# Kernel optimization log

Measured on AMD Instinct MI355X. Metric: run time of the kernel, lower is better.

Reference implementation:

```python
import jax, jax.numpy as jnp
import numpy as np

B, S, D, H = 4, 4096, 1024, 1024  # batch, seq, token_dim (d+1), hidden_dim
WIN, STRIDE, GLOB = 256, 128, 16
EPS = 1e-5
SCALE = 1.0 / np.sqrt(H).astype(np.float32)


def build_sparse_causal_mask(seq_len):
    i = jnp.arange(seq_len)[:, None]
    j = jnp.arange(seq_len)[None, :]
    causal = j <= i
    allowed = causal & ((i - j) < WIN)          # local window
    allowed = allowed | (((i - j) % STRIDE == 0) & causal)  # strided
    allowed = allowed | ((j < GLOB) & causal)   # global tokens
    return allowed  # [S, S] bool


def layer_norm(x, g, b):
    m = jnp.mean(x, axis=-1, keepdims=True)
    v = jnp.mean(jnp.square(x - m), axis=-1, keepdims=True)
    return (x - m) * jax.lax.rsqrt(v + EPS) * g + b


def setup_inputs() -> dict:
    key = jax.random.key(0)
    ks = jax.random.split(key, 5)
    gain = 0.01
    # xavier_uniform bound for square [H,D] matrices
    def xavier(k, shape):
        bound = gain * np.sqrt(6.0 / (shape[0] + shape[1]))
        return jax.random.uniform(k, shape, jnp.float32, -bound, bound)
    return {
        "tokens": jax.random.normal(ks[0], (B, S, D), jnp.float32),
        "Wq": xavier(ks[1], (D, H)),
        "Wk": xavier(ks[2], (D, H)),
        "Wv": xavier(ks[3], (D, D)),
        "Wo": xavier(ks[4], (D, D)),
        "g1": jnp.ones((D,), jnp.float32),
        "b1": jnp.zeros((D,), jnp.float32),
        "g2": jnp.ones((D,), jnp.float32),
        "b2": jnp.zeros((D,), jnp.float32),
    }


def reference(tokens, Wq, Wk, Wv, Wo, g1, b1, g2, b2):
    x = layer_norm(tokens, g1, b1)                    # [B,S,D]
    Q = jnp.einsum("bsd,dh->bsh", x, Wq)              # [B,S,H]
    K = jnp.einsum("bsd,dh->bsh", x, Wk)
    V = jnp.einsum("bsd,de->bse", x, Wv)              # [B,S,D]
    scores = jnp.einsum("bqh,bkh->bqk", Q, K) * SCALE  # [B,S,S]
    allowed = build_sparse_causal_mask(S)
    scores = jnp.where(allowed, scores, -jnp.inf)
    weights = jax.nn.softmax(scores, axis=-1)
    attn = jnp.einsum("bqk,bkd->bqd", weights, V)     # [B,S,D]
    out = tokens + jnp.einsum("bsd,de->bse", attn, Wo) * 0.1
    return layer_norm(out, g2, b2)
```

## Files before the change

kernel.cpp:

```cpp
#include <hip/hip_runtime.h>

#define S_LEN   4096
#define D_DIM   1024
#define WIN_    256
#define STRIDE_ 128
#define GLOB_   16
#define SCALE_F 0.03125f
#define EPS_F   1e-5f

typedef __bf16 bf16x8 __attribute__((ext_vector_type(8)));
typedef float  f32x4  __attribute__((ext_vector_type(4)));

__device__ __forceinline__ float b2f(unsigned short u) {
    union { unsigned int i; float f; } c; c.i = ((unsigned int)u) << 16; return c.f;
}
__device__ __forceinline__ unsigned short f2bf(float f) {
    union { float f; unsigned int i; } c; c.f = f;
    unsigned int u = c.i;
    u += 0x7fffu + ((u >> 16) & 1u);
    return (unsigned short)(u >> 16);
}

__device__ __forceinline__ void gld_lds16(const void* g, void* l) {
    __builtin_amdgcn_global_load_lds(
        (const __attribute__((address_space(1))) unsigned int*)g,
        (__attribute__((address_space(3))) unsigned int*)l, 16, 0, 0);
}

__device__ __forceinline__ float blk_sum(float v, float* red, int tid) {
    int lane = tid & 63, wv = tid >> 6;
    #pragma unroll
    for (int m = 32; m >= 1; m >>= 1) v += __shfl_xor(v, m, 64);
    __syncthreads();
    if (lane == 0) red[wv] = v;
    __syncthreads();
    return red[0] + red[1] + red[2] + red[3];
}

__global__ __launch_bounds__(256) void ln_full_kernel(
    const float* __restrict__ in, float* __restrict__ mu, float* __restrict__ rs,
    const float* __restrict__ g, const float* __restrict__ bb,
    unsigned short* __restrict__ xb) {
    __shared__ float red[4];
    int row = blockIdx.x, tid = threadIdx.x;
    size_t off = (size_t)row * D_DIM + tid * 4;
    float4 r = *(const float4*)(in + off);
    float s = blk_sum(r.x + r.y + r.z + r.w, red, tid);
    float mean = s * (1.0f / 1024.0f);
    float d0 = r.x - mean, d1 = r.y - mean, d2 = r.z - mean, d3 = r.w - mean;
    float s2 = blk_sum(d0*d0 + d1*d1 + d2*d2 + d3*d3, red, tid);
    float rstd = rsqrtf(s2 * (1.0f / 1024.0f) + EPS_F);
    if (tid == 0) { mu[row] = mean; rs[row] = rstd; }
    float4 gr = *(const float4*)(g  + tid * 4);
    float4 br = *(const float4*)(bb + tid * 4);
    ushort4 o;
    o.x = f2bf(d0 * rstd * gr.x + br.x);
    o.y = f2bf(d1 * rstd * gr.y + br.y);
    o.z = f2bf(d2 * rstd * gr.z + br.z);
    o.w = f2bf(d3 * rstd * gr.w + br.w);
    *(ushort4*)(xb + off) = o;
}

__global__ __launch_bounds__(256) void ln2_inplace_kernel(
    float* __restrict__ data, const float* __restrict__ g,
    const float* __restrict__ bb) {
    __shared__ float red[4];
    int row = blockIdx.x, tid = threadIdx.x;
    size_t off = (size_t)row * D_DIM + tid * 4;
    float4 v = *(const float4*)(data + off);
    float s = blk_sum(v.x + v.y + v.z + v.w, red, tid);
    float mean = s * (1.0f / 1024.0f);
    float d0 = v.x - mean, d1 = v.y - mean, d2 = v.z - mean, d3 = v.w - mean;
    float s2 = blk_sum(d0*d0 + d1*d1 + d2*d2 + d3*d3, red, tid);
    float rstd = rsqrtf(s2 * (1.0f / 1024.0f) + EPS_F);
    float4 gr = *(const float4*)(g  + tid * 4);
    float4 br = *(const float4*)(bb + tid * 4);
    float4 o;
    o.x = d0 * rstd * gr.x + br.x;
    o.y = d1 * rstd * gr.y + br.y;
    o.z = d2 * rstd * gr.z + br.z;
    o.w = d3 * rstd * gr.w + br.w;
    *(float4*)(data + off) = o;
}

__global__ __launch_bounds__(256) void transpose_cvt(
    const float* __restrict__ in, unsigned short* __restrict__ outp) {
    __shared__ unsigned short tile[32][33];
    int tid = threadIdx.x;
    int tx = tid & 31, ty = tid >> 5;
    int bx = blockIdx.x * 32, by = blockIdx.y * 32;
    #pragma unroll
    for (int r = 0; r < 32; r += 8)
        tile[ty + r][tx] = f2bf(in[(size_t)(by + ty + r) * 1024 + bx + tx]);
    __syncthreads();
    #pragma unroll
    for (int r = 0; r < 32; r += 8)
        outp[(size_t)(bx + ty + r) * 1024 + by + tx] = tile[tx][ty + r];
}

__global__ __launch_bounds__(256) void transpose1024(
    const unsigned short* __restrict__ in, unsigned short* __restrict__ outp) {
    __shared__ unsigned short tile[32][33];
    int tid = threadIdx.x;
    int tx = tid & 31, ty = tid >> 5;
    int bx = blockIdx.x * 32, by = blockIdx.y * 32;
    #pragma unroll
    for (int r = 0; r < 32; r += 8)
        tile[ty + r][tx] = in[(size_t)(by + ty + r) * 1024 + bx + tx];
    __syncthreads();
    #pragma unroll
    for (int r = 0; r < 32; r += 8)
        outp[(size_t)(bx + ty + r) * 1024 + by + tx] = tile[tx][ty + r];
}

__global__ __launch_bounds__(256) void transln16_kernel(
    const float* __restrict__ tok, const float* __restrict__ mu,
    const float* __restrict__ rs, const float* __restrict__ g,
    const float* __restrict__ bb, unsigned short* __restrict__ X16) {
    __shared__ unsigned short Lt[32][36];
    int tid = threadIdx.x;
    int tx = tid & 31, ty = tid >> 5;
    int s0 = blockIdx.x * 32;
    int n0 = blockIdx.y * 32;
    int b  = blockIdx.z;
    float gv = g[n0 + tx], bv = bb[n0 + tx];
    #pragma unroll
    for (int r = 0; r < 32; r += 8) {
        int grow = (b << 12) + s0 + ty + r;
        float v = tok[(size_t)grow * 1024 + n0 + tx];
        Lt[tx][ty + r] = f2bf((v - mu[grow]) * rs[grow] * gv + bv);
    }
    __syncthreads();
    int tt  = tid >> 6;
    int sTl = tt >> 1, nTl = tt & 1;
    int idx = tid & 63;
    int nl  = idx >> 2, so4 = (idx & 3) << 2;
    uint2 v = *(const uint2*)&Lt[nTl * 16 + nl][sTl * 16 + so4];
    size_t off = (size_t)b * 4194304 +
        (((size_t)(((s0 >> 4) + sTl) * 64 + (n0 >> 4) + nTl)) << 8) +
        (nl << 4) + so4;
    *(uint2*)(X16 + off) = v;
}

__global__ __launch_bounds__(256) void gemm_small(
    const float* __restrict__ A32, const float* __restrict__ W32,
    unsigned short* __restrict__ C16) {
    const int K = 1024, N = 1024;
    __shared__ __align__(16) unsigned short As[64][40];
    __shared__ __align__(16) unsigned short Bs[64][40];
    int tid  = threadIdx.x;
    int lane = tid & 63, wv = tid >> 6;
    int lm   = lane & 15, quad = lane >> 4;
    int m0 = blockIdx.y * 64, n0 = blockIdx.x * 64;
    int srow = tid >> 2, scg = tid & 3;
    int bk   = tid >> 3, bn  = (tid & 7) * 8;

    f32x4 acc[4] = {};
    for (int k0 = 0; k0 < K; k0 += 32) {
        const float* ap = A32 + (size_t)(m0 + srow) * K + k0 + scg * 8;
        float4 p = *(const float4*)(ap);
        float4 q = *(const float4*)(ap + 4);
        union { uint4 u; unsigned short s[8]; } w;
        w.s[0]=f2bf(p.x); w.s[1]=f2bf(p.y); w.s[2]=f2bf(p.z); w.s[3]=f2bf(p.w);
        w.s[4]=f2bf(q.x); w.s[5]=f2bf(q.y); w.s[6]=f2bf(q.z); w.s[7]=f2bf(q.w);
        *(uint4*)&As[srow][scg * 8] = w.u;

        const float* wp = W32 + (size_t)(k0 + bk) * N + n0 + bn;
        float4 a = *(const float4*)wp, b = *(const float4*)(wp + 4);
        float wvv[8] = {a.x,a.y,a.z,a.w,b.x,b.y,b.z,b.w};
        #pragma unroll
        for (int e = 0; e < 8; ++e) Bs[bn + e][bk] = f2bf(wvv[e]);
        __syncthreads();
        bf16x8 af = *(const bf16x8*)&As[wv * 16 + lm][quad * 8];
        #pragma unroll
        for (int t = 0; t < 4; ++t) {
            bf16x8 bfr = *(const bf16x8*)&Bs[t * 16 + lm][quad * 8];
            acc[t] = __builtin_amdgcn_mfma_f32_16x16x32_bf16(af, bfr, acc[t], 0, 0, 0);
        }
        __syncthreads();
    }
    #pragma unroll
    for (int t = 0; t < 4; ++t) {
        int col = n0 + t * 16 + lm;
        #pragma unroll
        for (int r = 0; r < 4; ++r) {
            int row = m0 + wv * 16 + quad * 4 + r;
            C16[(size_t)row * N + col] = f2bf(acc[t][r]);
        }
    }
}

template <bool EPI>
__global__ __launch_bounds__(256) void gemm128(
    const unsigned short* __restrict__ A, const unsigned short* __restrict__ BT,
    unsigned short* __restrict__ C16, float* __restrict__ Cres,
    const float* __restrict__ tok) {
    const int K = 1024, N = 1024;
    __shared__ __align__(16) unsigned short As[4096];
    __shared__ __align__(16) unsigned short Bs[4096];
    int tid = threadIdx.x, lane = tid & 63, wv = tid >> 6;
    int lm = lane & 15, quad = lane >> 4;
    int wr = wv >> 1, wc = wv & 1;
    int flat = blockIdx.y * 8 + blockIdx.x;
    int logical = ((flat & 7) << 7) | (flat >> 3);
    int m0 = (logical >> 3) * 128, n0 = (logical & 7) * 128;

    f32x4 acc[4][4] = {};

    const unsigned short* ga0 = A  + (size_t)(m0 + lane) * K + wv * 8;
    const unsigned short* ga1 = A  + (size_t)(m0 + 64 + lane) * K + wv * 8;
    const unsigned short* gb0 = BT + (size_t)(n0 + lane) * K + wv * 8;
    const unsigned short* gb1 = BT + (size_t)(n0 + 64 + lane) * K + wv * 8;
    unsigned short* la0 = &As[wv * 1024 + lane * 8];
    unsigned short* la1 = &As[wv * 1024 + 512 + lane * 8];
    unsigned short* lb0 = &Bs[wv * 1024 + lane * 8];
    unsigned short* lb1 = &Bs[wv * 1024 + 512 + lane * 8];

    for (int k0 = 0; k0 < K; k0 += 32) {
        gld_lds16(ga0 + k0, la0);
        gld_lds16(ga1 + k0, la1);
        gld_lds16(gb0 + k0, lb0);
        gld_lds16(gb1 + k0, lb1);
        __syncthreads();
        bf16x8 af[4], bfr[4];
        #pragma unroll
        for (int t = 0; t < 4; ++t) {
            af[t]  = *(const bf16x8*)&As[quad * 1024 + (wr * 64 + t * 16 + lm) * 8];
            bfr[t] = *(const bf16x8*)&Bs[quad * 1024 + (wc * 64 + t * 16 + lm) * 8];
        }
        #pragma unroll
        for (int mt = 0; mt < 4; ++mt)
            #pragma unroll
            for (int nt = 0; nt < 4; ++nt)
                acc[mt][nt] = __builtin_amdgcn_mfma_f32_16x16x32_bf16(
                    af[mt], bfr[nt], acc[mt][nt], 0, 0, 0);
        __syncthreads();
    }
    #pragma unroll
    for (int mt = 0; mt < 4; ++mt) {
        #pragma unroll
        for (int nt = 0; nt < 4; ++nt) {
            int col = n0 + wc * 64 + nt * 16 + lm;
            #pragma unroll
            for (int r = 0; r < 4; ++r) {
                int row = m0 + wr * 64 + mt * 16 + quad * 4 + r;
                size_t idx = (size_t)row * N + col;
                if (EPI) Cres[idx] = tok[idx] + 0.1f * acc[mt][nt][r];
                else     C16[idx]  = f2bf(acc[mt][nt][r]);
            }
        }
    }
}

#define NT_MAX 48
#define SCROW  776
__global__ __launch_bounds__(256) void attn16_kernel(
    const unsigned short* __restrict__ Q, const unsigned short* __restrict__ K,
    const unsigned short* __restrict__ XT, unsigned short* __restrict__ Ao) {
    __shared__ __align__(16) unsigned short Ps[16 * SCROW];
    int tid = threadIdx.x, lane = tid & 63, wv = tid >> 6;
    int lm = lane & 15, quad = lane >> 4;
    int bxr = blockIdx.x;
    int xcd = bxr & 7;
    int sl  = bxr >> 3;
    int batch = xcd >> 1;
    int ptyp  = xcd & 1;
    int t = ptyp ? (64 + sl)
                 : ((sl < 64) ? sl : (128 + sl));
    int bx = batch * 256 + t;
    int b  = bx >> 8;
    int i0 = (bx & 255) << 4;
    int rowbase = (b << 12) + i0;
    int wlo = i0 - 256; if (wlo < 0) wlo = 0;
    int nwin = ((i0 - wlo) >> 4) + 1;
    int tmax = (i0 - 16) / 128;
    int nstr = tmax - 2; if (nstr < 0) nstr = 0;
    int nglob = (wlo > 0) ? 1 : 0;
    int ntiles = nwin + nstr + nglob;
    int ntp = (ntiles + 3) & ~3;

    const unsigned short* Qg = Q + (size_t)(rowbase + lm) * 1024 + quad * 8;

    const unsigned short* Kbp = K + (((size_t)b << 12) << 10);
    for (int tg = wv * 4; tg < ntp; tg += 16) {
        f32x4 acc[4] = {};
        int tb[4];
        #pragma unroll
        for (int c = 0; c < 4; ++c) {
            int t = tg + c, base = 0;
            if (t < nwin) base = wlo + (t << 4);
            else if (t - nwin < nstr) base = i0 - 128 * (3 + (t - nwin));
            tb[c] = base;
        }
        for (int k0 = 0; k0 < 1024; k0 += 32) {
            bf16x8 a = *(const bf16x8*)(Qg + k0);
            #pragma unroll
            for (int c = 0; c < 4; ++c) {
                bf16x8 bb = *(const bf16x8*)(Kbp +
                    (size_t)(tb[c] + lm) * 1024 + k0 + quad * 8);
                acc[c] = __builtin_amdgcn_mfma_f32_16x16x32_bf16(a, bb, acc[c], 0, 0, 0);
            }
        }
        #pragma unroll
        for (int c = 0; c < 4; ++c) {
            int t = tg + c;
            int j = tb[c] + lm;
            bool pad = (t >= ntiles);
            #pragma unroll
            for (int r = 0; r < 4; ++r) {
                int i = i0 + quad * 4 + r;
                int diff = i - j;
                bool ok = !pad && (j <= i) &&
                          (diff < 256 || (diff & 127) == 0 || j < 16);
                Ps[(quad * 4 + r) * SCROW + (t << 4) + lm] =
                    f2bf(ok ? acc[c][r] : -1e30f);
            }
        }
    }
    __syncthreads();

    int ncol = ntp << 4;
    for (int q = wv * 4; q < wv * 4 + 4; ++q) {
        unsigned short* row = &Ps[q * SCROW];
        float mx = -1e30f;
        for (int c = lane; c < ncol; c += 64) mx = fmaxf(mx, b2f(row[c]));
        #pragma unroll
        for (int m = 32; m >= 1; m >>= 1) mx = fmaxf(mx, __shfl_xor(mx, m, 64));
        float sm = 0.f;
        for (int c = lane; c < ncol; c += 64)
            sm += __expf(SCALE_F * (b2f(row[c]) - mx));
        #pragma unroll
        for (int m = 32; m >= 1; m >>= 1) sm += __shfl_xor(sm, m, 64);
        float inv = 1.0f / sm;
        for (int c = lane; c < ncol; c += 64)
            row[c] = f2bf(__expf(SCALE_F * (b2f(row[c]) - mx)) * inv);
    }
    __syncthreads();

    int n0w = wv * 256;
    int nT0 = wv << 4;
    const unsigned short* Xb = XT + (size_t)b * 4194304;
    int octet = quad & 1, tsel = quad >> 1;
    f32x4 oacc[16] = {};
    int nch = ntp >> 1;
    for (int c = 0; c < nch; ++c) {
        int t0 = 2 * c, t1 = 2 * c + 1;
        int b0 = (t0 < nwin) ? wlo + (t0 << 4)
               : ((t0 - nwin < nstr) ? i0 - 128 * (3 + t0 - nwin) : 0);
        int b1 = (t1 < nwin) ? wlo + (t1 << 4)
               : ((t1 - nwin < nstr) ? i0 - 128 * (3 + t1 - nwin) : 0);
        bf16x8 a = *(const bf16x8*)&Ps[lm * SCROW + (c << 5) + quad * 8];
        int sT = (tsel ? b1 : b0) >> 4;
        const unsigned short* xp = Xb + (((size_t)(sT * 64 + nT0)) << 8)
                                      + (lm << 4) + (octet << 3);
        #pragma unroll
        for (int nt = 0; nt < 16; ++nt) {
            bf16x8 bb2 = *(const bf16x8*)(xp + (nt << 8));
            oacc[nt] = __builtin_amdgcn_mfma_f32_16x16x32_bf16(a, bb2, oacc[nt], 0, 0, 0);
        }
    }
    #pragma unroll
    for (int nt = 0; nt < 16; ++nt) {
        int col = n0w + nt * 16 + lm;
        #pragma unroll
        for (int r = 0; r < 4; ++r) {
            int row = rowbase + quad * 4 + r;
            Ao[(size_t)row * 1024 + col] = f2bf(oacc[nt][r]);
        }
    }
}

extern "C" void kernel_launch(void* const* d_in, const int* in_sizes, int n_in,
                              void* d_out, int out_size, void* d_ws, size_t ws_size,
                              hipStream_t stream) {
    const float* tokens = (const float*)d_in[0];
    const float* Wq = (const float*)d_in[1];
    const float* Wk = (const float*)d_in[2];
    const float* Wv = (const float*)d_in[3];
    const float* Wo = (const float*)d_in[4];
    const float* g1 = (const float*)d_in[5];
    const float* b1 = (const float*)d_in[6];
    const float* g2 = (const float*)d_in[7];
    const float* b2 = (const float*)d_in[8];
    float* out = (float*)d_out;
    char* ws = (char*)d_ws;

    const size_t MB = 1048576;
    float* mu = (float*)(ws);
    float* rs = (float*)(ws + 65536);
    unsigned short* WqT    = (unsigned short*)(ws + 1 * MB);
    unsigned short* WkT    = (unsigned short*)(ws + 3 * MB);
    unsigned short* Wfused = (unsigned short*)(ws + 5 * MB);
    unsigned short* WfT    = (unsigned short*)(ws + 7 * MB);
    unsigned short* Qb     = (unsigned short*)(ws + 9 * MB);
    unsigned short* xb     = (unsigned short*)d_out;
    unsigned short* X16    = (unsigned short*)d_out;
    unsigned short* Kb     = (unsigned short*)d_out + 16777216;
    unsigned short* attnX  = Qb;

    dim3 b256(256);
    const int ROWS = 4 * S_LEN;
    dim3 tg(32, 32);
    dim3 gsmall(16, 16);
    dim3 g128(8, 128);
    dim3 gtl(128, 32, 4);

    ln_full_kernel<<<ROWS, b256, 0, stream>>>(tokens, mu, rs, g1, b1, xb);
    transpose_cvt<<<tg, b256, 0, stream>>>(Wq, WqT);
    transpose_cvt<<<tg, b256, 0, stream>>>(Wk, WkT);
    gemm_small<<<gsmall, b256, 0, stream>>>(Wv, Wo, Wfused);
    transpose1024<<<tg, b256, 0, stream>>>(Wfused, WfT);
    gemm128<false><<<g128, b256, 0, stream>>>(xb, WqT, Qb, nullptr, nullptr);
    gemm128<false><<<g128, b256, 0, stream>>>(xb, WkT, Kb, nullptr, nullptr);
    transln16_kernel<<<gtl, b256, 0, stream>>>(tokens, mu, rs, g1, b1, X16);
    attn16_kernel<<<1024, b256, 0, stream>>>(Qb, Kb, X16, attnX);
    gemm128<true><<<g128, b256, 0, stream>>>(attnX, WfT, nullptr, out, tokens);
    ln2_inplace_kernel<<<ROWS, b256, 0, stream>>>(out, g2, b2);
}
```

Before: 668.1 us.

## Double-buffer GEMM LDS tiles and software-prefetch attention operands with MFMA priority

The GEMM kernel now uses two LDS buffers per operand, so the loads for the next k-slice are issued before the MFMAs on the current slice, and only one barrier remains per iteration. The QK^T score loop register-prefetches the next Q and K fragments one step ahead. s_setprio raises wave priority around the MFMA blocks in the GEMM, the score loop and the PV loop. The goal is to hide global-load latency behind matrix math, at the cost of doubled LDS use and more live registers, which could reduce occupancy.

New measurement: 786.8 us. +17.8%, slower.

```diff
diff --git a/kernel.cpp b/kernel.cpp
--- a/kernel.cpp
+++ b/kernel.cpp
@@ -196,8 +196,8 @@
     unsigned short* __restrict__ C16, float* __restrict__ Cres,
     const float* __restrict__ tok) {
     const int K = 1024, N = 1024;
-    __shared__ __align__(16) unsigned short As[4096];
-    __shared__ __align__(16) unsigned short Bs[4096];
+    __shared__ __align__(16) unsigned short As[2][4096];
+    __shared__ __align__(16) unsigned short Bs[2][4096];
     int tid = threadIdx.x, lane = tid & 63, wv = tid >> 6;
     int lm = lane & 15, quad = lane >> 4;
     int wr = wv >> 1, wc = wv & 1;
@@ -211,30 +211,40 @@
     const unsigned short* ga1 = A  + (size_t)(m0 + 64 + lane) * K + wv * 8;
     const unsigned short* gb0 = BT + (size_t)(n0 + lane) * K + wv * 8;
     const unsigned short* gb1 = BT + (size_t)(n0 + 64 + lane) * K + wv * 8;
-    unsigned short* la0 = &As[wv * 1024 + lane * 8];
-    unsigned short* la1 = &As[wv * 1024 + 512 + lane * 8];
-    unsigned short* lb0 = &Bs[wv * 1024 + lane * 8];
-    unsigned short* lb1 = &Bs[wv * 1024 + 512 + lane * 8];
-
-    for (int k0 = 0; k0 < K; k0 += 32) {
-        gld_lds16(ga0 + k0, la0);
-        gld_lds16(ga1 + k0, la1);
-        gld_lds16(gb0 + k0, lb0);
-        gld_lds16(gb1 + k0, lb1);
-        __syncthreads();
+    int lof0 = wv * 1024 + lane * 8;
+    int lof1 = wv * 1024 + 512 + lane * 8;
+
+    gld_lds16(ga0, &As[0][lof0]);
+    gld_lds16(ga1, &As[0][lof1]);
+    gld_lds16(gb0, &Bs[0][lof0]);
+    gld_lds16(gb1, &Bs[0][lof1]);
+    __syncthreads();
+
+    int cur = 0;
+    for (int t = 0; t < 32; ++t) {
+        if (t + 1 < 32) {
+            int kn = (t + 1) * 32, nb = cur ^ 1;
+            gld_lds16(ga0 + kn, &As[nb][lof0]);
+            gld_lds16(ga1 + kn, &As[nb][lof1]);
+            gld_lds16(gb0 + kn, &Bs[nb][lof0]);
+            gld_lds16(gb1 + kn, &Bs[nb][lof1]);
+        }
         bf16x8 af[4], bfr[4];
         #pragma unroll
-        for (int t = 0; t < 4; ++t) {
-            af[t]  = *(const bf16x8*)&As[quad * 1024 + (wr * 64 + t * 16 + lm) * 8];
-            bfr[t] = *(const bf16x8*)&Bs[quad * 1024 + (wc * 64 + t * 16 + lm) * 8];
-        }
+        for (int q = 0; q < 4; ++q) {
+            af[q]  = *(const bf16x8*)&As[cur][quad * 1024 + (wr * 64 + q * 16 + lm) * 8];
+            bfr[q] = *(const bf16x8*)&Bs[cur][quad * 1024 + (wc * 64 + q * 16 + lm) * 8];
+        }
+        __builtin_amdgcn_s_setprio(1);
         #pragma unroll
         for (int mt = 0; mt < 4; ++mt)
             #pragma unroll
             for (int nt = 0; nt < 4; ++nt)
                 acc[mt][nt] = __builtin_amdgcn_mfma_f32_16x16x32_bf16(
                     af[mt], bfr[nt], acc[mt][nt], 0, 0, 0);
+        __builtin_amdgcn_s_setprio(0);
         __syncthreads();
+        cur ^= 1;
     }
     #pragma unroll
     for (int mt = 0; mt < 4; ++mt) {
@@ -292,14 +302,31 @@
             else if (t - nwin < nstr) base = i0 - 128 * (3 + (t - nwin));
             tb[c] = base;
         }
+        const unsigned short* kp0 = Kbp + (size_t)(tb[0] + lm) * 1024 + quad * 8;
+        const unsigned short* kp1 = Kbp + (size_t)(tb[1] + lm) * 1024 + quad * 8;
+        const unsigned short* kp2 = Kbp + (size_t)(tb[2] + lm) * 1024 + quad * 8;
+        const unsigned short* kp3 = Kbp + (size_t)(tb[3] + lm) * 1024 + quad * 8;
+        bf16x8 a_n  = *(const bf16x8*)(Qg);
+        bf16x8 b_n0 = *(const bf16x8*)(kp0);
+        bf16x8 b_n1 = *(const bf16x8*)(kp1);
+        bf16x8 b_n2 = *(const bf16x8*)(kp2);
+        bf16x8 b_n3 = *(const bf16x8*)(kp3);
         for (int k0 = 0; k0 < 1024; k0 += 32) {
-            bf16x8 a = *(const bf16x8*)(Qg + k0);
-            #pragma unroll
-            for (int c = 0; c < 4; ++c) {
-                bf16x8 bb = *(const bf16x8*)(Kbp +
-                    (size_t)(tb[c] + lm) * 1024 + k0 + quad * 8);
-                acc[c] = __builtin_amdgcn_mfma_f32_16x16x32_bf16(a, bb, acc[c], 0, 0, 0);
+            bf16x8 a_c = a_n, b_c0 = b_n0, b_c1 = b_n1, b_c2 = b_n2, b_c3 = b_n3;
+            int kn = k0 + 32;
+            if (kn < 1024) {
+                a_n  = *(const bf16x8*)(Qg + kn);
+                b_n0 = *(const bf16x8*)(kp0 + kn);
+                b_n1 = *(const bf16x8*)(kp1 + kn);
+                b_n2 = *(const bf16x8*)(kp2 + kn);
+                b_n3 = *(const bf16x8*)(kp3 + kn);
             }
+            __builtin_amdgcn_s_setprio(1);
+            acc[0] = __builtin_amdgcn_mfma_f32_16x16x32_bf16(a_c, b_c0, acc[0], 0, 0, 0);
+            acc[1] = __builtin_amdgcn_mfma_f32_16x16x32_bf16(a_c, b_c1, acc[1], 0, 0, 0);
+            acc[2] = __builtin_amdgcn_mfma_f32_16x16x32_bf16(a_c, b_c2, acc[2], 0, 0, 0);
+            acc[3] = __builtin_amdgcn_mfma_f32_16x16x32_bf16(a_c, b_c3, acc[3], 0, 0, 0);
+            __builtin_amdgcn_s_setprio(0);
         }
         #pragma unroll
         for (int c = 0; c < 4; ++c) {
@@ -353,11 +380,13 @@
         int sT = (tsel ? b1 : b0) >> 4;
         const unsigned short* xp = Xb + (((size_t)(sT * 64 + nT0)) << 8)
                                       + (lm << 4) + (octet << 3);
+        __builtin_amdgcn_s_setprio(1);
         #pragma unroll
         for (int nt = 0; nt < 16; ++nt) {
             bf16x8 bb2 = *(const bf16x8*)(xp + (nt << 8));
             oacc[nt] = __builtin_amdgcn_mfma_f32_16x16x32_bf16(a, bb2, oacc[nt], 0, 0, 0);
         }
+        __builtin_amdgcn_s_setprio(0);
     }
     #pragma unroll
     for (int nt = 0; nt < 16; ++nt) {
```
